# Kernel optimization log

Hardware: AMD Instinct MI355X
Metric: run time of the kernel (lower is better)

## Reference

```python
import math
import jax, jax.numpy as jnp
import numpy as np

B, S, D = 4, 2048, 1024
N_HEAD = 16


def setup_inputs() -> dict:
    key = jax.random.key(0)
    k1, k2 = jax.random.split(key)
    x = jax.random.normal(k1, (B, S, D), dtype=jnp.float32)
    # xavier-uniform style scale for the fused QKV kernel
    limit = math.sqrt(6.0 / (D + 3 * D))
    W_qkv = jax.random.uniform(k2, (D, 3 * D), dtype=jnp.float32, minval=-limit, maxval=limit)
    b_qkv = jnp.zeros((3 * D,), dtype=jnp.float32)
    return {"x": x, "W_qkv": W_qkv, "b_qkv": b_qkv}


def reference(x, W_qkv, b_qkv):
    batch_size, seq_len, d_model = x.shape
    head_dim = d_model // N_HEAD
    # fused QKV projection: [B, S, 3D]
    qkv = jnp.einsum('bsd,de->bse', x, W_qkv) + b_qkv
    qkv = qkv.reshape(batch_size, seq_len, N_HEAD, 3 * head_dim)
    qkv = qkv.transpose(0, 2, 1, 3)  # [B, H, S, 3*hd]
    q, k, v = jnp.split(qkv, 3, axis=-1)
    # scaled dot-product attention with causal mask
    attn_logits = jnp.einsum('bhqd,bhkd->bhqk', q, k) / math.sqrt(head_dim)
    causal = jnp.tril(jnp.ones((seq_len, seq_len), dtype=jnp.float32))[None, None]
    attn_logits = jnp.where(causal == 0, -jnp.inf, attn_logits)
    attn = jax.nn.softmax(attn_logits, axis=-1)
    out = jnp.einsum('bhqk,bhkd->bhqd', attn, v)  # [B, H, S, hd]
    out = out.transpose(0, 2, 1, 3).reshape(batch_size, seq_len, -1)
    return out
```

## Files before the change

### kernel.cpp

```cpp
#include <hip/hip_runtime.h>
#include <hip/hip_bf16.h>
#include <cstdint>

typedef __bf16 bf16x8 __attribute__((ext_vector_type(8)));
typedef float f32x4 __attribute__((ext_vector_type(4)));
typedef float f32x16 __attribute__((ext_vector_type(16)));

__device__ inline unsigned short f2bf(float f) {
    union { float f; unsigned int u; } v; v.f = f;
    unsigned int u = v.u;
    unsigned int r = (u + 0x7FFFu + ((u >> 16) & 1u)) >> 16;
    return (unsigned short)r;
}

__device__ inline f32x4 mfma16(bf16x8 a, bf16x8 b, f32x4 c) {
    return __builtin_amdgcn_mfma_f32_16x16x32_bf16(a, b, c, 0, 0, 0);
}

__device__ inline f32x16 mfma32(bf16x8 a, bf16x8 b, f32x16 c) {
    return __builtin_amdgcn_mfma_f32_32x32x16_bf16(a, b, c, 0, 0, 0);
}

__device__ inline bf16x8 ldfrag(const unsigned short* p) {
    uint4 v = *(const uint4*)p;
    return __builtin_bit_cast(bf16x8, v);
}

__device__ inline void cp16(const unsigned short* g, unsigned short* l) {
    __builtin_amdgcn_global_load_lds(
        (const __attribute__((address_space(1))) unsigned int*)g,
        (__attribute__((address_space(3))) unsigned int*)l,
        16, 0, 0);
}

__device__ inline unsigned int pkbf(float a, float b) {
    return __builtin_amdgcn_perm(__builtin_bit_cast(unsigned int, b),
                                 __builtin_bit_cast(unsigned int, a),
                                 0x07060302u);
}

__device__ inline void plswap(unsigned int& a, unsigned int& b) {
    typedef unsigned int u32x2 __attribute__((ext_vector_type(2)));
    u32x2 r = __builtin_amdgcn_permlane32_swap(a, b, false, false);
    a = r[0]; b = r[1];
}

__global__ void k_convert_x(const float* __restrict__ in,
                            unsigned short* __restrict__ out, int n4) {
    int i = blockIdx.x * blockDim.x + threadIdx.x;
    if (i < n4) {
        float4 f = ((const float4*)in)[i];
        ushort4 o;
        o.x = f2bf(f.x); o.y = f2bf(f.y); o.z = f2bf(f.z); o.w = f2bf(f.w);
        ((ushort4*)out)[i] = o;
    }
}

__global__ void k_transpose_w(const float* __restrict__ W,
                              unsigned short* __restrict__ Wt) {
    __shared__ float tile[32][33];
    int nt = blockIdx.x, kt = blockIdx.y;
    int tx = threadIdx.x & 31, ty = threadIdx.x >> 5;
#pragma unroll
    for (int yy = 0; yy < 4; ++yy) {
        int y = ty + yy * 8;
        tile[y][tx] = W[(size_t)(kt * 32 + y) * 3072 + nt * 32 + tx];
    }
    __syncthreads();
#pragma unroll
    for (int yy = 0; yy < 4; ++yy) {
        int nrow = ty + yy * 8;
        Wt[(size_t)(nt * 32 + nrow) * 1024 + kt * 32 + tx] = f2bf(tile[tx][nrow]);
    }
}

__global__ __launch_bounds__(256) void k_qkv_gemm(
    const unsigned short* __restrict__ A,
    const unsigned short* __restrict__ Bt,
    const float* __restrict__ bias,
    unsigned short* __restrict__ C) {
    __shared__ unsigned short As[128 * 32];
    __shared__ unsigned short Bs[128 * 32];
    const int tid = threadIdx.x;
    const int lane = tid & 63;
    const int w = tid >> 6;
    const int wm = w >> 1, wn = w & 1;
    const int l15 = lane & 15;
    const int quad = lane >> 4;
    const int m0 = blockIdx.y * 128;
    const int n0 = blockIdx.x * 128;

    f32x4 acc[4][4] = {};

    for (int k0 = 0; k0 < 1024; k0 += 32) {
#pragma unroll
        for (int i = 0; i < 2; ++i) {
            int c = tid + i * 256;
            int row = c >> 2, seg = c & 3;
            cp16(A + (size_t)(m0 + row) * 1024 + k0 + seg * 8, &As[c * 8]);
            cp16(Bt + (size_t)(n0 + row) * 1024 + k0 + seg * 8, &Bs[c * 8]);
        }
        __syncthreads();
        const int col8 = quad * 8;
        bf16x8 af[4], bfr[4];
#pragma unroll
        for (int i = 0; i < 4; ++i)
            af[i] = ldfrag(As + (wm * 64 + i * 16 + l15) * 32 + col8);
#pragma unroll
        for (int j = 0; j < 4; ++j)
            bfr[j] = ldfrag(Bs + (wn * 64 + j * 16 + l15) * 32 + col8);
#pragma unroll
        for (int i = 0; i < 4; ++i)
#pragma unroll
            for (int j = 0; j < 4; ++j)
                acc[i][j] = mfma16(af[i], bfr[j], acc[i][j]);
        __syncthreads();
    }
#pragma unroll
    for (int i = 0; i < 4; ++i) {
#pragma unroll
        for (int j = 0; j < 4; ++j) {
            int col = n0 + wn * 64 + j * 16 + l15;
            float bv = bias[col];
#pragma unroll
            for (int r = 0; r < 4; ++r) {
                int row = m0 + wm * 64 + i * 16 + quad * 4 + r;
                C[(size_t)row * 3072 + col] = f2bf(acc[i][j][r] + bv);
            }
        }
    }
}

__global__ __launch_bounds__(256) void k_transpose_v(
    const unsigned short* __restrict__ qkv,
    unsigned short* __restrict__ VtG) {
    __shared__ unsigned short t[64][65];
    const int st = blockIdx.x;
    const int h = blockIdx.y;
    const int b = blockIdx.z;
    const int tid = threadIdx.x;
    const int voff = h * 192 + 128;
    const size_t base = (size_t)b * 2048 * 3072;
#pragma unroll
    for (int i = 0; i < 2; ++i) {
        int c = tid + i * 256;
        int row = c >> 3, seg = c & 7;
        uint4 v = *(const uint4*)(qkv + base + (size_t)(st * 64 + row) * 3072 + voff + seg * 8);
        unsigned short u8[8];
        *(uint4*)u8 = v;
#pragma unroll
        for (int u = 0; u < 8; ++u) t[row][seg * 8 + u] = u8[u];
    }
    __syncthreads();
    const size_t obase = ((size_t)(b * 16 + h) * 64) * 2048 + st * 64;
#pragma unroll
    for (int i = 0; i < 2; ++i) {
        int c = tid + i * 256;
        int drow = c >> 3, seg = c & 7;
        unsigned short u8[8];
#pragma unroll
        for (int u = 0; u < 8; ++u) u8[u] = t[seg * 8 + u][drow];
        *(uint4*)(VtG + obase + (size_t)drow * 2048 + seg * 8) = *(uint4*)u8;
    }
}

__global__ __launch_bounds__(256) void k_attn(
    const unsigned short* __restrict__ qkv,
    const unsigned short* __restrict__ VtG,
    float* __restrict__ out) {
    const int p = blockIdx.x;
    const int hb = p & 63;
    const int h = hb & 15;
    const int b = hb >> 4;
    const int qt = 31 - (p >> 6);
    const int tid = threadIdx.x;
    const int lane = tid & 63;
    const int w = tid >> 6;
    const int wm = w >> 1;
    const int wn = w & 1;
    const int l31 = lane & 31;
    const int hi = lane >> 5;

    __shared__ __align__(16) unsigned short KsF[2 * 64 * 64];
    __shared__ __align__(16) unsigned short VsF[2 * 64 * 64];

    const size_t base = (size_t)b * 2048 * 3072;
    const int qoff = h * 192, koff = h * 192 + 64;
    const size_t vtbase = (size_t)(b * 16 + h) * 64 * 2048;

    const int srow0 = tid >> 3, sseg = tid & 7;
    const int gsw = (sseg ^ (srow0 & 7)) * 8;
    unsigned short* kd0 = &KsF[tid * 8];
    unsigned short* kd1 = &KsF[2048 + tid * 8];
    unsigned short* vd0 = &VsF[tid * 8];
    unsigned short* vd1 = &VsF[2048 + tid * 8];

    const int xr7 = l31 & 7;
    const int kfbase = (32 * wm + l31) * 64;
    const int vfb0 = l31 * 64;
    const int vfb1 = (32 + l31) * 64;
    const int qcol = 32 * wn + l31;

    const float sc = 0.125f * 1.44269504088896340736f;

    const int qrow = qt * 64 + qcol;
    const unsigned short* qp = qkv + base + (size_t)qrow * 3072 + qoff + hi * 8;
    bf16x8 bq[4];
#pragma unroll
    for (int t = 0; t < 4; ++t) bq[t] = ldfrag(qp + t * 16);

    const unsigned short* kp0 = qkv + base + koff + (size_t)srow0 * 3072 + gsw;
    const unsigned short* kp1 = kp0 + (size_t)32 * 3072;
    const unsigned short* vp0 = VtG + vtbase + (size_t)srow0 * 2048 + gsw;
    const unsigned short* vp1 = vp0 + (size_t)32 * 2048;

    f32x16 acc0 = {0,0,0,0,0,0,0,0,0,0,0,0,0,0,0,0};
    f32x16 acc1 = {0,0,0,0,0,0,0,0,0,0,0,0,0,0,0,0};
    float ptot = 0.f;

    cp16(kp0, kd0); cp16(kp1, kd1); cp16(vp0, vd0); cp16(vp1, vd1);
    __syncthreads();

    for (int kt = 0; kt <= qt; ++kt) {
        const int bo = (kt & 1) * 4096;
        const int bn = bo ^ 4096;
        if (kt < qt) {
            kp0 += 64 * 3072; kp1 += 64 * 3072;
            vp0 += 64;        vp1 += 64;
            cp16(kp0, kd0 + bn); cp16(kp1, kd1 + bn);
            cp16(vp0, vd0 + bn); cp16(vp1, vd1 + bn);
        }

        f32x16 s = {0,0,0,0,0,0,0,0,0,0,0,0,0,0,0,0};
#pragma unroll
        for (int t = 0; t < 4; ++t) {
            const unsigned short* ka =
                &KsF[bo + kfbase + ((2 * t + hi) ^ xr7) * 8];
            s = mfma32(ldfrag(ka), bq[t], s);
        }

        if (kt == qt) {
#pragma unroll
            for (int r = 0; r < 16; ++r) {
                const int srow = 32 * wm + (r & 3) + 8 * (r >> 2) + 4 * hi;
                if (srow > qcol) s[r] = -3.0e38f;
            }
        }

        float pvv[16];
#pragma unroll
        for (int r = 0; r < 16; ++r) {
            pvv[r] = __builtin_amdgcn_exp2f(
                __builtin_fmaf(s[r], sc, -16.0f));
            ptot += pvv[r];
        }
        unsigned int pk0 = pkbf(pvv[0], pvv[1]),   pk1 = pkbf(pvv[2], pvv[3]);
        unsigned int pk2 = pkbf(pvv[4], pvv[5]),   pk3 = pkbf(pvv[6], pvv[7]);
        unsigned int pk4 = pkbf(pvv[8], pvv[9]),   pk5 = pkbf(pvv[10], pvv[11]);
        unsigned int pk6 = pkbf(pvv[12], pvv[13]), pk7 = pkbf(pvv[14], pvv[15]);
        plswap(pk0, pk2); plswap(pk1, pk3);
        plswap(pk4, pk6); plswap(pk5, pk7);
        uint4 w0; w0.x = pk0; w0.y = pk1; w0.z = pk2; w0.w = pk3;
        uint4 w1; w1.x = pk4; w1.y = pk5; w1.z = pk6; w1.w = pk7;
        const bf16x8 pf0 = __builtin_bit_cast(bf16x8, w0);
        const bf16x8 pf1 = __builtin_bit_cast(bf16x8, w1);

        const int su0 = ((4 * wm + hi) ^ xr7) * 8;
        const int su1 = ((4 * wm + 2 + hi) ^ xr7) * 8;
        acc0 = mfma32(ldfrag(&VsF[bo + vfb0 + su0]), pf0, acc0);
        acc0 = mfma32(ldfrag(&VsF[bo + vfb0 + su1]), pf1, acc0);
        acc1 = mfma32(ldfrag(&VsF[bo + vfb1 + su0]), pf0, acc1);
        acc1 = mfma32(ldfrag(&VsF[bo + vfb1 + su1]), pf1, acc1);

        __syncthreads();
    }

    float* Sc = (float*)KsF;
    float* Pt = (float*)VsF;
    const int lb = (wn * 64 + lane) * 8;
    if (wm == 1) {
#pragma unroll
        for (int g = 0; g < 4; ++g) {
            float4 v;
            v.x = acc0[g * 4 + 0]; v.y = acc0[g * 4 + 1];
            v.z = acc0[g * 4 + 2]; v.w = acc0[g * 4 + 3];
            ((float4*)Sc)[lb + (g ^ (lane & 7))] = v;
        }
#pragma unroll
        for (int g = 0; g < 4; ++g) {
            float4 v;
            v.x = acc1[g * 4 + 0]; v.y = acc1[g * 4 + 1];
            v.z = acc1[g * 4 + 2]; v.w = acc1[g * 4 + 3];
            ((float4*)Sc)[lb + ((g + 4) ^ (lane & 7))] = v;
        }
        Pt[wn * 64 + lane] = ptot;
    }
    __syncthreads();
    if (wm == 0) {
#pragma unroll
        for (int g = 0; g < 4; ++g) {
            float4 v = ((const float4*)Sc)[lb + (g ^ (lane & 7))];
            acc0[g * 4 + 0] += v.x; acc0[g * 4 + 1] += v.y;
            acc0[g * 4 + 2] += v.z; acc0[g * 4 + 3] += v.w;
        }
#pragma unroll
        for (int g = 0; g < 4; ++g) {
            float4 v = ((const float4*)Sc)[lb + ((g + 4) ^ (lane & 7))];
            acc1[g * 4 + 0] += v.x; acc1[g * 4 + 1] += v.y;
            acc1[g * 4 + 2] += v.z; acc1[g * 4 + 3] += v.w;
        }
        float l = ptot + Pt[wn * 64 + lane];
        l += __shfl_xor(l, 32, 64);
        const float inv = __builtin_amdgcn_rcpf(l);
        float* op = out + ((size_t)b * 2048 + qrow) * 1024 + h * 64 + 4 * hi;
#pragma unroll
        for (int g = 0; g < 4; ++g) {
            float4 v;
            v.x = acc0[g * 4 + 0] * inv; v.y = acc0[g * 4 + 1] * inv;
            v.z = acc0[g * 4 + 2] * inv; v.w = acc0[g * 4 + 3] * inv;
            *(float4*)(op + g * 8) = v;
        }
#pragma unroll
        for (int g = 0; g < 4; ++g) {
            float4 v;
            v.x = acc1[g * 4 + 0] * inv; v.y = acc1[g * 4 + 1] * inv;
            v.z = acc1[g * 4 + 2] * inv; v.w = acc1[g * 4 + 3] * inv;
            *(float4*)(op + 32 + g * 8) = v;
        }
    }
}

extern "C" void kernel_launch(void* const* d_in, const int* in_sizes, int n_in,
                              void* d_out, int out_size, void* d_ws, size_t ws_size,
                              hipStream_t stream) {
    const float* x = (const float*)d_in[0];
    const float* W = (const float*)d_in[1];
    const float* bq = (const float*)d_in[2];
    float* out = (float*)d_out;

    unsigned short* xbf = (unsigned short*)d_ws;
    unsigned short* wtbf = xbf + (size_t)8192 * 1024;
    unsigned short* qkvbf = wtbf + (size_t)3072 * 1024;
    unsigned short* VtG = xbf;

    k_convert_x<<<8192, 256, 0, stream>>>(x, xbf, 8192 * 1024 / 4);
    k_transpose_w<<<dim3(96, 32), 256, 0, stream>>>(W, wtbf);
    k_qkv_gemm<<<dim3(24, 64), 256, 0, stream>>>(xbf, wtbf, bq, qkvbf);
    k_transpose_v<<<dim3(32, 16, 4), 256, 0, stream>>>(qkvbf, VtG);
    k_attn<<<2048, 256, 0, stream>>>(qkvbf, VtG, out);
}
```

Measured before the change: 222.9 us.

## Triple-buffer QKV GEMM with 256x128 tiles, 32x32 MFMA and swizzled LDS

Rewrites the QKV projection GEMM to use 512-thread blocks computing 256x128 tiles with a 64-wide K step. Global-to-LDS copies are triple-buffered, with manual vmcnt waits so loads overlap MFMA work. Fragments are read from an XOR-swizzled LDS layout to avoid bank conflicts, and 32x32x16 MFMAs replace 16x16x32 ones. The goal is more data reuse per tile and less load latency exposed in the GEMM stage. In exchange it uses about 147KB of LDS per block, which limits occupancy to one block per CU.

```diff
diff --git a/kernel.cpp b/kernel.cpp
--- a/kernel.cpp
+++ b/kernel.cpp
@@ -74,59 +74,96 @@
     }
 }
 
-__global__ __launch_bounds__(256) void k_qkv_gemm(
+__global__ __launch_bounds__(512, 2) void k_qkv_gemm(
     const unsigned short* __restrict__ A,
     const unsigned short* __restrict__ Bt,
     const float* __restrict__ bias,
     unsigned short* __restrict__ C) {
-    __shared__ unsigned short As[128 * 32];
-    __shared__ unsigned short Bs[128 * 32];
+    __shared__ __align__(16) unsigned short As[3 * 256 * 64];
+    __shared__ __align__(16) unsigned short Bs[3 * 128 * 64];
     const int tid = threadIdx.x;
     const int lane = tid & 63;
     const int w = tid >> 6;
     const int wm = w >> 1, wn = w & 1;
-    const int l15 = lane & 15;
-    const int quad = lane >> 4;
-    const int m0 = blockIdx.y * 128;
+    const int l31 = lane & 31;
+    const int hi = lane >> 5;
+    const int xr7 = l31 & 7;
+    const int m0 = blockIdx.y * 256;
     const int n0 = blockIdx.x * 128;
 
-    f32x4 acc[4][4] = {};
-
-    for (int k0 = 0; k0 < 1024; k0 += 32) {
-#pragma unroll
-        for (int i = 0; i < 2; ++i) {
-            int c = tid + i * 256;
-            int row = c >> 2, seg = c & 3;
-            cp16(A + (size_t)(m0 + row) * 1024 + k0 + seg * 8, &As[c * 8]);
-            cp16(Bt + (size_t)(n0 + row) * 1024 + k0 + seg * 8, &Bs[c * 8]);
-        }
-        __syncthreads();
-        const int col8 = quad * 8;
-        bf16x8 af[4], bfr[4];
+    const int srow = tid >> 3, sseg = tid & 7;
+    const int gsw = (sseg ^ (srow & 7)) * 8;
+    const unsigned short* pA = A + (size_t)(m0 + srow) * 1024 + gsw;
+    const unsigned short* pB = Bt + (size_t)(n0 + srow) * 1024 + gsw;
+
+    f32x16 acc[2][2] = {};
+
+    auto stage = [&](int buf, int k0) {
+        unsigned short* da = &As[buf * 16384 + tid * 8];
+        unsigned short* db = &Bs[buf * 8192 + tid * 8];
 #pragma unroll
         for (int i = 0; i < 4; ++i)
-            af[i] = ldfrag(As + (wm * 64 + i * 16 + l15) * 32 + col8);
-#pragma unroll
-        for (int j = 0; j < 4; ++j)
-            bfr[j] = ldfrag(Bs + (wn * 64 + j * 16 + l15) * 32 + col8);
-#pragma unroll
-        for (int i = 0; i < 4; ++i)
-#pragma unroll
-            for (int j = 0; j < 4; ++j)
-                acc[i][j] = mfma16(af[i], bfr[j], acc[i][j]);
-        __syncthreads();
-    }
-#pragma unroll
-    for (int i = 0; i < 4; ++i) {
-#pragma unroll
-        for (int j = 0; j < 4; ++j) {
-            int col = n0 + wn * 64 + j * 16 + l15;
-            float bv = bias[col];
-#pragma unroll
-            for (int r = 0; r < 4; ++r) {
-                int row = m0 + wm * 64 + i * 16 + quad * 4 + r;
-                C[(size_t)row * 3072 + col] = f2bf(acc[i][j][r] + bv);
-            }
+            cp16(pA + (size_t)i * 64 * 1024 + k0, da + i * 4096);
+#pragma unroll
+        for (int j = 0; j < 2; ++j)
+            cp16(pB + (size_t)j * 64 * 1024 + k0, db + j * 4096);
+    };
+
+    stage(0, 0);
+    stage(1, 64);
+
+    for (int kt = 0; kt < 16; ++kt) {
+        const int buf = kt % 3;
+        if (kt == 15)
+            asm volatile("s_waitcnt vmcnt(0)" ::: "memory");
+        else
+            asm volatile("s_waitcnt vmcnt(6)" ::: "memory");
+        __builtin_amdgcn_s_barrier();
+        if (kt + 2 < 16) stage((kt + 2) % 3, (kt + 2) * 64);
+
+        const unsigned short* ab = &As[buf * 16384];
+        const unsigned short* bb = &Bs[buf * 8192];
+        bf16x8 af[2][4], bfr[2][4];
+#pragma unroll
+        for (int rb = 0; rb < 2; ++rb) {
+            const int r = wm * 64 + rb * 32 + l31;
+#pragma unroll
+            for (int ks = 0; ks < 4; ++ks)
+                af[rb][ks] = ldfrag(ab + r * 64 + ((ks * 2 + hi) ^ xr7) * 8);
+        }
+#pragma unroll
+        for (int cb = 0; cb < 2; ++cb) {
+            const int r = wn * 64 + cb * 32 + l31;
+#pragma unroll
+            for (int ks = 0; ks < 4; ++ks)
+                bfr[cb][ks] = ldfrag(bb + r * 64 + ((ks * 2 + hi) ^ xr7) * 8);
+        }
+#pragma unroll
+        for (int rb = 0; rb < 2; ++rb)
+#pragma unroll
+            for (int cb = 0; cb < 2; ++cb)
+#pragma unroll
+                for (int ks = 0; ks < 4; ++ks)
+                    acc[rb][cb] = mfma32(af[rb][ks], bfr[cb][ks], acc[rb][cb]);
+
+        asm volatile("s_waitcnt lgkmcnt(0)" ::: "memory");
+    }
+
+#pragma unroll
+    for (int cb = 0; cb < 2; ++cb) {
+        const int col = n0 + wn * 64 + cb * 32 + l31;
+        const float bv = bias[col];
+#pragma unroll
+        for (int rb = 0; rb < 2; ++rb) {
+            const int rbase = m0 + wm * 64 + rb * 32 + 4 * hi;
+#pragma unroll
+            for (int g = 0; g < 4; ++g)
+#pragma unroll
+                for (int rr = 0; rr < 4; ++rr) {
+                    const int row = rbase + g * 8 + rr;
+                    C[(size_t)row * 3072 + col] =
+                        f2bf(acc[rb][cb][g * 4 + rr] + bv);
+                }
         }
     }
 }
@@ -345,7 +382,7 @@
 
     k_convert_x<<<8192, 256, 0, stream>>>(x, xbf, 8192 * 1024 / 4);
     k_transpose_w<<<dim3(96, 32), 256, 0, stream>>>(W, wtbf);
-    k_qkv_gemm<<<dim3(24, 64), 256, 0, stream>>>(xbf, wtbf, bq, qkvbf);
+    k_qkv_gemm<<<dim3(24, 32), 512, 0, stream>>>(xbf, wtbf, bq, qkvbf);
     k_transpose_v<<<dim3(32, 16, 4), 256, 0, stream>>>(qkvbf, VtG);
     k_attn<<<2048, 256, 0, stream>>>(qkvbf, VtG, out);
 }
```

Result: no change. 224.8 us (+0.8%).
